# Kernel optimization log

Hardware: AMD Instinct MI355X
Metric: run time of the kernel (lower is better)

Reference implementation:

```python
import jax, jax.numpy as jnp
import numpy as np

HID = 128
CDIM = 128
NCH = 3
NDIM = 3


def _linear_params(key, fan_in, fan_out):
    kw, kb = jax.random.split(key)
    bound = 1.0 / np.sqrt(fan_in)
    W = jax.random.uniform(kw, (fan_in, fan_out), jnp.float32, -bound, bound)
    b = jax.random.uniform(kb, (fan_out,), jnp.float32, -bound, bound)
    return W, b


def setup_inputs() -> dict:
    key = jax.random.key(0)
    keys = jax.random.split(key, 12)
    p = jax.random.normal(keys[0], (32, 8192, NDIM), jnp.float32)
    W_pos, b_pos = _linear_params(keys[1], NDIM, 2 * HID)
    W0, b0 = _linear_params(keys[2], 2 * HID, HID)
    W1, b1 = _linear_params(keys[3], 2 * HID, HID)
    W2, b2 = _linear_params(keys[4], 2 * HID, HID)
    W3, b3 = _linear_params(keys[5], 2 * HID, HID)
    Wc, bc = _linear_params(keys[6], HID, CDIM)
    Wm0, bm0 = _linear_params(keys[7], CDIM, HID)
    Wm1, bm1 = _linear_params(keys[8], HID, HID)
    Wm2, bm2 = _linear_params(keys[9], HID, HID)
    Wp, bp = _linear_params(keys[10], HID, NCH * 3)
    return dict(p=p, W_pos=W_pos, b_pos=b_pos, W0=W0, b0=b0, W1=W1, b1=b1,
                W2=W2, b2=b2, W3=W3, b3=b3, Wc=Wc, bc=bc,
                Wm0=Wm0, bm0=bm0, Wm1=Wm1, bm1=bm1, Wm2=Wm2, bm2=bm2,
                Wp=Wp, bp=bp)


def _relu(x):
    return jnp.maximum(x, 0)


def _pool_cat(net):
    # max over points (dim=1), broadcast back and concat on features
    pooled = jnp.max(net, axis=1, keepdims=True)
    pooled = jnp.broadcast_to(pooled, net.shape)
    return jnp.concatenate([net, pooled], axis=2)  # [B, T, 2*hid]


def reference(p, W_pos, b_pos, W0, b0, W1, b1, W2, b2, W3, b3,
              Wc, bc, Wm0, bm0, Wm1, bm1, Wm2, bm2, Wp, bp):
    net = p @ W_pos + b_pos                      # [B, T, 2*hid]
    net = _relu(net) @ W0 + b0                   # [B, T, hid]
    net = _relu(_pool_cat(net)) @ W1 + b1        # [B, T, hid]
    net = _relu(_pool_cat(net)) @ W2 + b2        # [B, T, hid]
    net = _relu(_pool_cat(net)) @ W3 + b3        # [B, T, hid]
    net = jnp.max(net, axis=1)                   # [B, hid]
    net = _relu(net) @ Wc + bc                   # [B, c_dim]
    net = _relu(net) @ Wm0 + bm0
    net = _relu(net) @ Wm1 + bm1
    net = _relu(net) @ Wm2 + bm2
    net = _relu(net) @ Wp + bp                   # [B, n_channels*3]
    return net
```

## Files before the change

kernel.cpp:

```cpp
#include <hip/hip_runtime.h>


using bf16x8 = __attribute__((ext_vector_type(8))) __bf16;
using u16x8  = __attribute__((ext_vector_type(8))) unsigned short;
using f32x4  = __attribute__((ext_vector_type(4))) float;

__device__ __forceinline__ unsigned short f2bf(float x) {
  __bf16 b = (__bf16)x;
  return __builtin_bit_cast(unsigned short, b);
}

__device__ __forceinline__ f32x4 mfma16(bf16x8 a, bf16x8 b, f32x4 c) {
  return __builtin_amdgcn_mfma_f32_16x16x32_bf16(a, b, c, 0, 0, 0);
}

union FragU { unsigned short us[8]; u16x8 u; bf16x8 v; };

__global__ __launch_bounds__(256) void k_pack_all(
    const float* __restrict__ W0, const float* __restrict__ W1,
    const float* __restrict__ W2, const float* __restrict__ W3,
    unsigned short* __restrict__ Wt) {
  const int blk = blockIdx.x, t = threadIdx.x;
  const float* src; int slot; unsigned short* dst;
  if (blk < 16)      { src = W0; slot = blk * 256 + t;        dst = Wt; }
  else if (blk < 24) { src = W1; slot = (blk - 16) * 256 + t; dst = Wt + 32768; }
  else if (blk < 32) { src = W2; slot = (blk - 24) * 256 + t; dst = Wt + 49152; }
  else               { src = W3; slot = (blk - 32) * 256 + t; dst = Wt + 65536; }
  const int ks = slot >> 9, rem = slot & 511;
  const int nt = rem >> 6, lane = rem & 63;
  const int n = nt * 16 + (lane & 15);
  const int kb = ks * 32 + ((lane >> 4) << 3);
  FragU fr;
#pragma unroll
  for (int j = 0; j < 8; ++j) fr.us[j] = f2bf(src[(kb + j) * 128 + n]);
  reinterpret_cast<u16x8*>(dst)[slot] = fr.u;
}

__device__ __forceinline__ void epilogue256(
    unsigned short* hs, float (*pmaxs)[128], const f32x4 (&acc)[4][8],
    const float (&bias)[8], int t, int blk, unsigned short* __restrict__ h,
    float* __restrict__ pm, bool write_h) {
  const int w = t >> 6, lane = t & 63, g = lane >> 4, c = lane & 15;
  float colmax[8];
#pragma unroll
  for (int nt = 0; nt < 8; ++nt) colmax[nt] = 0.f;
#pragma unroll
  for (int mi = 0; mi < 4; ++mi) {
#pragma unroll
    for (int nt = 0; nt < 8; ++nt) {
#pragma unroll
      for (int r = 0; r < 4; ++r) {
        const float v = fmaxf(acc[mi][nt][r] + bias[nt], 0.f);
        colmax[nt] = fmaxf(colmax[nt], v);
        if (write_h)
          hs[(w * 64 + mi * 16 + g * 4 + r) * 136 + nt * 16 + c] = f2bf(v);
      }
    }
  }
#pragma unroll
  for (int nt = 0; nt < 8; ++nt) {
    colmax[nt] = fmaxf(colmax[nt], __shfl_xor(colmax[nt], 16, 64));
    colmax[nt] = fmaxf(colmax[nt], __shfl_xor(colmax[nt], 32, 64));
  }
  if (lane < 16) {
#pragma unroll
    for (int nt = 0; nt < 8; ++nt) pmaxs[w][nt * 16 + c] = colmax[nt];
  }
  __syncthreads();
  if (write_h) {
    u16x8* hout = reinterpret_cast<u16x8*>(h) + (size_t)blk * 4096;
#pragma unroll
    for (int i = 0; i < 16; ++i) {
      const int s = i * 256 + t;
      const int tl = s >> 8, ks = (s >> 6) & 3, lp = s & 63;
      const int row = tl * 16 + (lp & 15);
      const int c0 = ks * 32 + ((lp >> 4) << 3);
      hout[tl * 256 + ks * 64 + lp] =
          *reinterpret_cast<const u16x8*>(&hs[row * 136 + c0]);
    }
  }
  if (t < 128) {
    pm[(size_t)blk * 128 + t] = fmaxf(fmaxf(pmaxs[0][t], pmaxs[1][t]),
                                      fmaxf(pmaxs[2][t], pmaxs[3][t]));
  }
}

__global__ __launch_bounds__(256, 2) void k_layer0(
    const float* __restrict__ p, const float* __restrict__ Wpos,
    const float* __restrict__ bpos, const float* __restrict__ b0,
    const unsigned short* __restrict__ Wt0, unsigned short* __restrict__ h,
    float* __restrict__ pm) {
  __shared__ float wls[1024];
  __shared__ unsigned short hs[256 * 136];
  __shared__ float pmaxs[4][128];
  const int t = threadIdx.x, blk = blockIdx.x;
  for (int i = t; i < 1024; i += 256) wls[i] = (i < 768) ? Wpos[i] : bpos[i - 768];

  const int w = t >> 6, lane = t & 63, g = lane >> 4, c = lane & 15;
  float px[4], py[4], pz[4];
#pragma unroll
  for (int mi = 0; mi < 4; ++mi) {
    const int row = blk * 256 + (w * 4 + mi) * 16 + c;
    px[mi] = p[row * 3 + 0]; py[mi] = p[row * 3 + 1]; pz[mi] = p[row * 3 + 2];
  }
  float bias[8];
#pragma unroll
  for (int nt = 0; nt < 8; ++nt) bias[nt] = b0[nt * 16 + c];

  f32x4 acc[4][8];
#pragma unroll
  for (int mi = 0; mi < 4; ++mi)
#pragma unroll
    for (int nt = 0; nt < 8; ++nt) acc[mi][nt] = f32x4{0.f, 0.f, 0.f, 0.f};
  __syncthreads();

  const bf16x8* Bf = reinterpret_cast<const bf16x8*>(Wt0);
#pragma unroll
  for (int ks = 0; ks < 8; ++ks) {
    bf16x8 B[8];
#pragma unroll
    for (int nt = 0; nt < 8; ++nt) B[nt] = Bf[(ks * 8 + nt) * 64 + lane];
    FragU a[4];
    const int kb = ks * 32 + g * 8;
#pragma unroll
    for (int mi = 0; mi < 4; ++mi) {
#pragma unroll
      for (int half = 0; half < 2; ++half) {
        const int kq = kb + half * 4;
        const float4 w0 = *reinterpret_cast<const float4*>(&wls[kq]);
        const float4 w1 = *reinterpret_cast<const float4*>(&wls[256 + kq]);
        const float4 w2 = *reinterpret_cast<const float4*>(&wls[512 + kq]);
        const float4 bb = *reinterpret_cast<const float4*>(&wls[768 + kq]);
        a[mi].us[half * 4 + 0] = f2bf(fmaxf(bb.x + px[mi] * w0.x + py[mi] * w1.x + pz[mi] * w2.x, 0.f));
        a[mi].us[half * 4 + 1] = f2bf(fmaxf(bb.y + px[mi] * w0.y + py[mi] * w1.y + pz[mi] * w2.y, 0.f));
        a[mi].us[half * 4 + 2] = f2bf(fmaxf(bb.z + px[mi] * w0.z + py[mi] * w1.z + pz[mi] * w2.z, 0.f));
        a[mi].us[half * 4 + 3] = f2bf(fmaxf(bb.w + px[mi] * w0.w + py[mi] * w1.w + pz[mi] * w2.w, 0.f));
      }
    }
#pragma unroll
    for (int mi = 0; mi < 4; ++mi)
#pragma unroll
      for (int nt = 0; nt < 8; ++nt)
        acc[mi][nt] = mfma16(a[mi].v, B[nt], acc[mi][nt]);
  }
  epilogue256(hs, pmaxs, acc, bias, t, blk, h, pm, true);
}

__global__ __launch_bounds__(256, 2) void k_layer(
    const unsigned short* __restrict__ Wta, const float* __restrict__ cvec,
    unsigned short* __restrict__ h, float* __restrict__ pm, int write_h) {
  __shared__ unsigned short hs[256 * 136];
  __shared__ float pmaxs[4][128];
  const int t = threadIdx.x, blk = blockIdx.x;
  const int w = t >> 6, lane = t & 63, c = lane & 15;
  const int b = blk >> 5;

  float bias[8];
#pragma unroll
  for (int nt = 0; nt < 8; ++nt) bias[nt] = cvec[b * 128 + nt * 16 + c];

  f32x4 acc[4][8];
#pragma unroll
  for (int mi = 0; mi < 4; ++mi)
#pragma unroll
    for (int nt = 0; nt < 8; ++nt) acc[mi][nt] = f32x4{0.f, 0.f, 0.f, 0.f};

  const u16x8* hbase = reinterpret_cast<const u16x8*>(h) + (size_t)blk * 4096;
  const bf16x8* Bf = reinterpret_cast<const bf16x8*>(Wta);
#pragma unroll
  for (int ks = 0; ks < 4; ++ks) {
    bf16x8 B[8];
#pragma unroll
    for (int nt = 0; nt < 8; ++nt) B[nt] = Bf[(ks * 8 + nt) * 64 + lane];
    FragU a[4];
#pragma unroll
    for (int mi = 0; mi < 4; ++mi) a[mi].u = hbase[(w * 4 + mi) * 256 + ks * 64 + lane];
#pragma unroll
    for (int mi = 0; mi < 4; ++mi)
#pragma unroll
      for (int nt = 0; nt < 8; ++nt)
        acc[mi][nt] = mfma16(a[mi].v, B[nt], acc[mi][nt]);
  }
  epilogue256(hs, pmaxs, acc, bias, t, blk, h, pm, write_h != 0);
}

__global__ __launch_bounds__(256) void k_combine(
    const float* __restrict__ pm, const float* __restrict__ Wn,
    const float* __restrict__ bn, float* __restrict__ cout) {
  const int b = blockIdx.x, t = threadIdx.x;
  const int f = t & 127, half = t >> 7;
  __shared__ float part[2][128];
  __shared__ float rm[128];
  float m = 0.f;
  for (int i = half * 16; i < half * 16 + 16; ++i)
    m = fmaxf(m, pm[(size_t)(b * 32 + i) * 128 + f]);
  part[half][f] = m;
  __syncthreads();
  if (t < 128) rm[f] = fmaxf(part[0][f], part[1][f]);
  __syncthreads();
  float s = 0.f;
  for (int q = half * 64; q < half * 64 + 64; ++q)
    s += rm[q] * Wn[(128 + q) * 128 + f];
  part[half][f] = s;
  __syncthreads();
  if (t < 128) cout[b * 128 + f] = part[0][f] + part[1][f] + bn[f];
}

__global__ __launch_bounds__(256) void k_final(
    const float* __restrict__ pm3,
    const float* __restrict__ Wc,  const float* __restrict__ bc,
    const float* __restrict__ Wm0, const float* __restrict__ bm0,
    const float* __restrict__ Wm1, const float* __restrict__ bm1,
    const float* __restrict__ Wm2, const float* __restrict__ bm2,
    const float* __restrict__ Wp,  const float* __restrict__ bp,
    float* __restrict__ out) {
  const int b = blockIdx.x, t = threadIdx.x;
  const int f = t & 127, half = t >> 7;
  __shared__ float part[2][128];
  __shared__ float x[128];
  float m = 0.f;
  for (int i = half * 16; i < half * 16 + 16; ++i)
    m = fmaxf(m, pm3[(size_t)(b * 32 + i) * 128 + f]);
  part[half][f] = m;
  __syncthreads();
  if (t < 128) x[f] = fmaxf(part[0][f], part[1][f]);
  __syncthreads();

  const float* Ws[4] = {Wc, Wm0, Wm1, Wm2};
  const float* bs[4] = {bc, bm0, bm1, bm2};
#pragma unroll
  for (int L = 0; L < 4; ++L) {
    float s = 0.f;
    for (int q = half * 64; q < half * 64 + 64; ++q)
      s += x[q] * Ws[L][q * 128 + f];
    part[half][f] = s;
    __syncthreads();
    if (t < 128) x[f] = fmaxf(part[0][f] + part[1][f] + bs[L][f], 0.f);
    __syncthreads();
  }
  if (t < 9) {
    float s = bp[t];
    for (int q = 0; q < 128; ++q) s += x[q] * Wp[q * 9 + t];
    out[b * 9 + t] = s;
  }
}

extern "C" void kernel_launch(void* const* d_in, const int* in_sizes, int n_in,
                              void* d_out, int out_size, void* d_ws, size_t ws_size,
                              hipStream_t stream) {
  const float *p = nullptr, *Wpos = nullptr, *bpos = nullptr;
  const float *Wp = nullptr, *bp = nullptr;
  const float *W256[4] = {}; int nW256 = 0;
  const float *W128[4] = {}; int nW128 = 0;
  const float *B128[8] = {}; int nB128 = 0;
  for (int i = 0; i < n_in; ++i) {
    const float* q = (const float*)d_in[i];
    switch (in_sizes[i]) {
      case 786432: p = q; break;
      case 768:    Wpos = q; break;
      case 256:    bpos = q; break;
      case 1152:   Wp = q; break;
      case 9:      bp = q; break;
      case 32768:  if (nW256 < 4) W256[nW256++] = q; break;
      case 16384:  if (nW128 < 4) W128[nW128++] = q; break;
      case 128:    if (nB128 < 8) B128[nB128++] = q; break;
      default: break;
    }
  }
  const float *W0 = W256[0], *W1 = W256[1], *W2 = W256[2], *W3 = W256[3];
  const float *Wc = W128[0], *Wm0 = W128[1], *Wm1 = W128[2], *Wm2 = W128[3];
  const float *b0 = B128[0], *b1 = B128[1], *b2 = B128[2], *b3 = B128[3];
  const float *bc = B128[4], *bm0 = B128[5], *bm1 = B128[6], *bm2 = B128[7];
  float* out = (float*)d_out;

  char* ws = (char*)d_ws;
  float* pm = (float*)ws;
  float* cv = (float*)(ws + 524288);
  unsigned short* Wt = (unsigned short*)(ws + 524288 + 16384);
  unsigned short* Wt0 = Wt;
  unsigned short* Wt1 = Wt + 32768;
  unsigned short* Wt2 = Wt + 49152;
  unsigned short* Wt3 = Wt + 65536;
  unsigned short* h = Wt + 81920;

  k_pack_all<<<40, 256, 0, stream>>>(W0, W1, W2, W3, Wt);
  k_layer0<<<1024, 256, 0, stream>>>(p, Wpos, bpos, b0, Wt0, h, pm);
  k_combine<<<32, 256, 0, stream>>>(pm, W1, b1, cv);
  k_layer<<<1024, 256, 0, stream>>>(Wt1, cv, h, pm, 1);
  k_combine<<<32, 256, 0, stream>>>(pm, W2, b2, cv);
  k_layer<<<1024, 256, 0, stream>>>(Wt2, cv, h, pm, 1);
  k_combine<<<32, 256, 0, stream>>>(pm, W3, b3, cv);
  k_layer<<<1024, 256, 0, stream>>>(Wt3, cv, h, pm, 0);
  k_final<<<32, 256, 0, stream>>>(pm, Wc, bc, Wm0, bm0, Wm1, bm1, Wm2, bm2, Wp, bp, out);
}
```

Baseline: 163.3 us.

## Use 512-thread blocks with 2 M-tiles per wave and per-wave LDS epilogue

Each 256-row block now runs 8 waves of 32 rows instead of 4 waves of 64, which halves the accumulator registers per thread and targets 4 blocks per CU for higher occupancy. The epilogue stages each wave's 16-row tile through a small private LDS slice and writes it straight to global in fragment order, dropping the block-wide LDS buffer and its barrier before the store. B fragments are loaded per nt inside the MFMA loop instead of held in an array. The cost is more B-fragment loads per row of output, since each wave reuses B across only 2 M tiles.

```diff
diff --git a/kernel.cpp b/kernel.cpp
--- a/kernel.cpp
+++ b/kernel.cpp
@@ -36,27 +36,45 @@
   reinterpret_cast<u16x8*>(dst)[slot] = fr.u;
 }
 
-__device__ __forceinline__ void epilogue256(
-    unsigned short* hs, float (*pmaxs)[128], const f32x4 (&acc)[4][8],
+__device__ __forceinline__ void epilogue512(
+    unsigned short* hsw, float (*pmaxs)[128], const f32x4 (&acc)[2][8],
     const float (&bias)[8], int t, int blk, unsigned short* __restrict__ h,
     float* __restrict__ pm, bool write_h) {
   const int w = t >> 6, lane = t & 63, g = lane >> 4, c = lane & 15;
   float colmax[8];
 #pragma unroll
   for (int nt = 0; nt < 8; ++nt) colmax[nt] = 0.f;
-#pragma unroll
-  for (int mi = 0; mi < 4; ++mi) {
-#pragma unroll
-    for (int nt = 0; nt < 8; ++nt) {
-#pragma unroll
-      for (int r = 0; r < 4; ++r) {
-        const float v = fmaxf(acc[mi][nt][r] + bias[nt], 0.f);
-        colmax[nt] = fmaxf(colmax[nt], v);
-        if (write_h)
-          hs[(w * 64 + mi * 16 + g * 4 + r) * 136 + nt * 16 + c] = f2bf(v);
+
+  if (write_h) {
+    u16x8* hout = reinterpret_cast<u16x8*>(h) + (size_t)blk * 4096;
+#pragma unroll
+    for (int mi = 0; mi < 2; ++mi) {
+#pragma unroll
+      for (int nt = 0; nt < 8; ++nt) {
+#pragma unroll
+        for (int r = 0; r < 4; ++r) {
+          const float v = fmaxf(acc[mi][nt][r] + bias[nt], 0.f);
+          colmax[nt] = fmaxf(colmax[nt], v);
+          hsw[(g * 4 + r) * 136 + nt * 16 + c] = f2bf(v);
+        }
       }
-    }
-  }
+#pragma unroll
+      for (int s = 0; s < 4; ++s) {
+        const u16x8 val =
+            *reinterpret_cast<const u16x8*>(&hsw[(lane & 15) * 136 + s * 32 + 8 * g]);
+        hout[(w * 2 + mi) * 256 + s * 64 + lane] = val;
+      }
+    }
+  } else {
+#pragma unroll
+    for (int mi = 0; mi < 2; ++mi)
+#pragma unroll
+      for (int nt = 0; nt < 8; ++nt)
+#pragma unroll
+        for (int r = 0; r < 4; ++r)
+          colmax[nt] = fmaxf(colmax[nt], acc[mi][nt][r] + bias[nt]);
+  }
+
 #pragma unroll
   for (int nt = 0; nt < 8; ++nt) {
     colmax[nt] = fmaxf(colmax[nt], __shfl_xor(colmax[nt], 16, 64));
@@ -67,49 +85,39 @@
     for (int nt = 0; nt < 8; ++nt) pmaxs[w][nt * 16 + c] = colmax[nt];
   }
   __syncthreads();
-  if (write_h) {
-    u16x8* hout = reinterpret_cast<u16x8*>(h) + (size_t)blk * 4096;
-#pragma unroll
-    for (int i = 0; i < 16; ++i) {
-      const int s = i * 256 + t;
-      const int tl = s >> 8, ks = (s >> 6) & 3, lp = s & 63;
-      const int row = tl * 16 + (lp & 15);
-      const int c0 = ks * 32 + ((lp >> 4) << 3);
-      hout[tl * 256 + ks * 64 + lp] =
-          *reinterpret_cast<const u16x8*>(&hs[row * 136 + c0]);
-    }
-  }
   if (t < 128) {
-    pm[(size_t)blk * 128 + t] = fmaxf(fmaxf(pmaxs[0][t], pmaxs[1][t]),
-                                      fmaxf(pmaxs[2][t], pmaxs[3][t]));
-  }
-}
-
-__global__ __launch_bounds__(256, 2) void k_layer0(
+    float m = pmaxs[0][t];
+#pragma unroll
+    for (int i = 1; i < 8; ++i) m = fmaxf(m, pmaxs[i][t]);
+    pm[(size_t)blk * 128 + t] = m;
+  }
+}
+
+__global__ __launch_bounds__(512, 4) void k_layer0(
     const float* __restrict__ p, const float* __restrict__ Wpos,
     const float* __restrict__ bpos, const float* __restrict__ b0,
     const unsigned short* __restrict__ Wt0, unsigned short* __restrict__ h,
     float* __restrict__ pm) {
   __shared__ float wls[1024];
-  __shared__ unsigned short hs[256 * 136];
-  __shared__ float pmaxs[4][128];
+  __shared__ unsigned short HS[8 * 2176];
+  __shared__ float pmaxs[8][128];
   const int t = threadIdx.x, blk = blockIdx.x;
-  for (int i = t; i < 1024; i += 256) wls[i] = (i < 768) ? Wpos[i] : bpos[i - 768];
+  for (int i = t; i < 1024; i += 512) wls[i] = (i < 768) ? Wpos[i] : bpos[i - 768];
 
   const int w = t >> 6, lane = t & 63, g = lane >> 4, c = lane & 15;
-  float px[4], py[4], pz[4];
-#pragma unroll
-  for (int mi = 0; mi < 4; ++mi) {
-    const int row = blk * 256 + (w * 4 + mi) * 16 + c;
+  float px[2], py[2], pz[2];
+#pragma unroll
+  for (int mi = 0; mi < 2; ++mi) {
+    const int row = blk * 256 + (w * 2 + mi) * 16 + c;
     px[mi] = p[row * 3 + 0]; py[mi] = p[row * 3 + 1]; pz[mi] = p[row * 3 + 2];
   }
   float bias[8];
 #pragma unroll
   for (int nt = 0; nt < 8; ++nt) bias[nt] = b0[nt * 16 + c];
 
-  f32x4 acc[4][8];
-#pragma unroll
-  for (int mi = 0; mi < 4; ++mi)
+  f32x4 acc[2][8];
+#pragma unroll
+  for (int mi = 0; mi < 2; ++mi)
 #pragma unroll
     for (int nt = 0; nt < 8; ++nt) acc[mi][nt] = f32x4{0.f, 0.f, 0.f, 0.f};
   __syncthreads();
@@ -117,13 +125,10 @@
   const bf16x8* Bf = reinterpret_cast<const bf16x8*>(Wt0);
 #pragma unroll
   for (int ks = 0; ks < 8; ++ks) {
-    bf16x8 B[8];
-#pragma unroll
-    for (int nt = 0; nt < 8; ++nt) B[nt] = Bf[(ks * 8 + nt) * 64 + lane];
-    FragU a[4];
+    FragU a[2];
     const int kb = ks * 32 + g * 8;
 #pragma unroll
-    for (int mi = 0; mi < 4; ++mi) {
+    for (int mi = 0; mi < 2; ++mi) {
 #pragma unroll
       for (int half = 0; half < 2; ++half) {
         const int kq = kb + half * 4;
@@ -138,19 +143,20 @@
       }
     }
 #pragma unroll
-    for (int mi = 0; mi < 4; ++mi)
-#pragma unroll
-      for (int nt = 0; nt < 8; ++nt)
-        acc[mi][nt] = mfma16(a[mi].v, B[nt], acc[mi][nt]);
-  }
-  epilogue256(hs, pmaxs, acc, bias, t, blk, h, pm, true);
-}
-
-__global__ __launch_bounds__(256, 2) void k_layer(
+    for (int nt = 0; nt < 8; ++nt) {
+      const bf16x8 B = Bf[(ks * 8 + nt) * 64 + lane];
+      acc[0][nt] = mfma16(a[0].v, B, acc[0][nt]);
+      acc[1][nt] = mfma16(a[1].v, B, acc[1][nt]);
+    }
+  }
+  epilogue512(&HS[w * 2176], pmaxs, acc, bias, t, blk, h, pm, true);
+}
+
+__global__ __launch_bounds__(512, 4) void k_layer(
     const unsigned short* __restrict__ Wta, const float* __restrict__ cvec,
     unsigned short* __restrict__ h, float* __restrict__ pm, int write_h) {
-  __shared__ unsigned short hs[256 * 136];
-  __shared__ float pmaxs[4][128];
+  __shared__ unsigned short HS[8 * 2176];
+  __shared__ float pmaxs[8][128];
   const int t = threadIdx.x, blk = blockIdx.x;
   const int w = t >> 6, lane = t & 63, c = lane & 15;
   const int b = blk >> 5;
@@ -159,9 +165,9 @@
 #pragma unroll
   for (int nt = 0; nt < 8; ++nt) bias[nt] = cvec[b * 128 + nt * 16 + c];
 
-  f32x4 acc[4][8];
-#pragma unroll
-  for (int mi = 0; mi < 4; ++mi)
+  f32x4 acc[2][8];
+#pragma unroll
+  for (int mi = 0; mi < 2; ++mi)
 #pragma unroll
     for (int nt = 0; nt < 8; ++nt) acc[mi][nt] = f32x4{0.f, 0.f, 0.f, 0.f};
 
@@ -169,19 +175,17 @@
   const bf16x8* Bf = reinterpret_cast<const bf16x8*>(Wta);
 #pragma unroll
   for (int ks = 0; ks < 4; ++ks) {
-    bf16x8 B[8];
-#pragma unroll
-    for (int nt = 0; nt < 8; ++nt) B[nt] = Bf[(ks * 8 + nt) * 64 + lane];
-    FragU a[4];
-#pragma unroll
-    for (int mi = 0; mi < 4; ++mi) a[mi].u = hbase[(w * 4 + mi) * 256 + ks * 64 + lane];
-#pragma unroll
-    for (int mi = 0; mi < 4; ++mi)
-#pragma unroll
-      for (int nt = 0; nt < 8; ++nt)
-        acc[mi][nt] = mfma16(a[mi].v, B[nt], acc[mi][nt]);
-  }
-  epilogue256(hs, pmaxs, acc, bias, t, blk, h, pm, write_h != 0);
+    FragU a0, a1;
+    a0.u = hbase[(w * 2 + 0) * 256 + ks * 64 + lane];
+    a1.u = hbase[(w * 2 + 1) * 256 + ks * 64 + lane];
+#pragma unroll
+    for (int nt = 0; nt < 8; ++nt) {
+      const bf16x8 B = Bf[(ks * 8 + nt) * 64 + lane];
+      acc[0][nt] = mfma16(a0.v, B, acc[0][nt]);
+      acc[1][nt] = mfma16(a1.v, B, acc[1][nt]);
+    }
+  }
+  epilogue512(&HS[w * 2176], pmaxs, acc, bias, t, blk, h, pm, write_h != 0);
 }
 
 __global__ __launch_bounds__(256) void k_combine(
@@ -284,12 +288,12 @@
   unsigned short* h = Wt + 81920;
 
   k_pack_all<<<40, 256, 0, stream>>>(W0, W1, W2, W3, Wt);
-  k_layer0<<<1024, 256, 0, stream>>>(p, Wpos, bpos, b0, Wt0, h, pm);
+  k_layer0<<<1024, 512, 0, stream>>>(p, Wpos, bpos, b0, Wt0, h, pm);
   k_combine<<<32, 256, 0, stream>>>(pm, W1, b1, cv);
-  k_layer<<<1024, 256, 0, stream>>>(Wt1, cv, h, pm, 1);
+  k_layer<<<1024, 512, 0, stream>>>(Wt1, cv, h, pm, 1);
   k_combine<<<32, 256, 0, stream>>>(pm, W2, b2, cv);
-  k_layer<<<1024, 256, 0, stream>>>(Wt2, cv, h, pm, 1);
+  k_layer<<<1024, 512, 0, stream>>>(Wt2, cv, h, pm, 1);
   k_combine<<<32, 256, 0, stream>>>(pm, W3, b3, cv);
-  k_layer<<<1024, 256, 0, stream>>>(Wt3, cv, h, pm, 0);
+  k_layer<<<1024, 512, 0, stream>>>(Wt3, cv, h, pm, 0);
   k_final<<<32, 256, 0, stream>>>(pm, Wc, bc, Wm0, bm0, Wm1, bm1, Wm2, bm2, Wp, bp, out);
 }
```

After: 160.3 us. Within noise of the previous version (-1.8%).
